# Performance work log

Hardware: AMD Instinct MI355X
Metric: run time of the kernel (lower is better)

## Reference

```python
import jax, jax.numpy as jnp
import numpy as np
import math

B, L, D, MAXL = 4, 4096, 1024, 16384


def setup_inputs() -> dict:
    key = jax.random.key(0)
    ks = jax.random.split(key, 12)
    s = 0.02
    def w(k, shape):
        return jax.random.normal(k, shape, jnp.float32) * s
    return {
        "x": jax.random.normal(ks[0], (B, L, D), jnp.float32),
        "pos_phases": jax.random.normal(ks[1], (MAXL, D), jnp.float32) * math.pi,
        "Wpv": w(ks[2], (D, D)), "bpv": jnp.zeros((D,), jnp.float32),
        "Wk": w(ks[3], (D, D)), "bk": jnp.zeros((D,), jnp.float32),
        "Wkv": w(ks[4], (D, D)), "bkv": jnp.zeros((D,), jnp.float32),
        "Wg1": w(ks[5], (2 * D, D)), "bg1": jnp.zeros((D,), jnp.float32),
        "Wg2": w(ks[6], (D, 1)), "bg2": jnp.zeros((1,), jnp.float32),
        "Wb1": w(ks[7], (D, D // 2)), "bb1": jnp.zeros((D // 2,), jnp.float32),
        "Wb2": w(ks[8], (D // 2, 2)), "bb2": jnp.zeros((2,), jnp.float32),
        "ln_g": jnp.ones((D,), jnp.float32), "ln_b": jnp.zeros((D,), jnp.float32),
        "Wo": w(ks[9], (D, D)), "bo": jnp.zeros((D,), jnp.float32),
    }


def _shift1(a):
    # torch.roll(a, 1, dims=1) with a[:, 0] = 0
    return jnp.concatenate([jnp.zeros_like(a[:, :1]), a[:, :-1]], axis=1)


def reference(x, pos_phases, Wpv, bpv, Wk, bk, Wkv, bkv, Wg1, bg1, Wg2, bg2,
              Wb1, bb1, Wb2, bb2, ln_g, ln_b, Wo, bo):
    Bq, Lq, Dq = x.shape
    sqrtD = jnp.sqrt(jnp.float32(Dq))

    # positional phasor memory
    pp = pos_phases[:Lq]                      # [L, D]
    pos_cos, pos_sin = jnp.cos(pp), jnp.sin(pp)
    pos_values = x @ Wpv + bpv                # [B, L, D]
    pos_mem_cos = jnp.cumsum(pos_cos * pos_values, axis=1)
    pos_mem_sin = jnp.cumsum(pos_sin * pos_values, axis=1)
    pos_ret = (pos_cos * pos_mem_cos + pos_sin * pos_mem_sin) / sqrtD

    # key-value phasor memory
    key_ph = jnp.tanh(x @ Wk + bk) * jnp.pi
    key_cos, key_sin = jnp.cos(key_ph), jnp.sin(key_ph)
    kv_values = x @ Wkv + bkv

    x_shifted = _shift1(x)
    gate_in = jnp.concatenate([x, x_shifted], axis=-1)       # [B, L, 2D]
    gh = jax.nn.gelu(gate_in @ Wg1 + bg1, approximate=False)
    value_gates = jax.nn.sigmoid(gh @ Wg2 + bg2)             # [B, L, 1]

    kc_s = _shift1(key_cos)
    ks_s = _shift1(key_sin)
    kv_mem_cos = jnp.cumsum(kc_s * kv_values * value_gates, axis=1)
    kv_mem_sin = jnp.cumsum(ks_s * kv_values * value_gates, axis=1)
    gate_cumsum = jnp.maximum(jnp.cumsum(value_gates, axis=1), 1.0)
    kv_ret = (key_cos * kv_mem_cos + key_sin * kv_mem_sin) / (jnp.sqrt(gate_cumsum) * sqrtD)

    # blend
    bh = jax.nn.gelu(x @ Wb1 + bb1, approximate=False)
    bw = jax.nn.softmax(bh @ Wb2 + bb2, axis=-1)             # [B, L, 2]
    blended = bw[..., 0:1] * pos_ret + bw[..., 1:2] * kv_ret

    # to_out: LayerNorm then Linear
    mu = jnp.mean(blended, axis=-1, keepdims=True)
    var = jnp.var(blended, axis=-1, keepdims=True)
    ln = (blended - mu) / jnp.sqrt(var + 1e-5) * ln_g + ln_b
    return x + ln @ Wo + bo
```

## Files before the change

### kernel.cpp

```cpp
#include <hip/hip_runtime.h>
#include <hip/hip_bf16.h>
#include <math.h>

using bf16 = __hip_bfloat16;
typedef __bf16 v8bf __attribute__((ext_vector_type(8)));
typedef float v4f __attribute__((ext_vector_type(4)));

#define B_ 4
#define L_ 4096
#define D_ 1024
#define M_ (B_*L_)
#define CCH 128
#define LCH (L_/CCH)
#define NF 3584

__device__ __forceinline__ float bf2f(bf16 v){ return __bfloat162float(v); }
__device__ __forceinline__ bf16 f2bf(float v){ return __float2bfloat16(v); }
__device__ __forceinline__ float us2f(ushort u){ union{unsigned u32; float f;}c; c.u32=((unsigned)u)<<16; return c.f; }
__device__ __forceinline__ ushort f2us(float v){ bf16 h=__float2bfloat16(v); return *(ushort*)&h; }
__device__ __forceinline__ float h2f(ushort u){ union{ushort s; _Float16 h;}c; c.s=u; return (float)c.h; }
__device__ __forceinline__ ushort f2h(float v){ union{ushort s; _Float16 h;}c; c.h=(_Float16)v; return c.s; }

__device__ __forceinline__ void g2l16(const void* g, void* l){
  __builtin_amdgcn_global_load_lds(
    (const __attribute__((address_space(1))) unsigned int*)g,
    (__attribute__((address_space(3))) unsigned int*)l, 16, 0, 0);
}

__global__ void k_zeroN(float* __restrict__ p, int n){
  int i = blockIdx.x*256 + threadIdx.x;
  if (i < n) p[i] = 0.0f;
}

__global__ void k_cvt(const float* __restrict__ in, bf16* __restrict__ out){
  int i = (blockIdx.x*256 + threadIdx.x)*4;
  float4 v = *(const float4*)(in + i);
  out[i]   = f2bf(v.x);
  out[i+1] = f2bf(v.y);
  out[i+2] = f2bf(v.z);
  out[i+3] = f2bf(v.w);
}

__global__ void k_cvt_pp(const float* __restrict__ in, ushort* __restrict__ out){
  int i = (blockIdx.x*256 + threadIdx.x)*4;
  float4 v = *(const float4*)(in + i);
  out[i]   = f2h(v.x);
  out[i+1] = f2h(v.y);
  out[i+2] = f2h(v.z);
  out[i+3] = f2h(v.w);
}

__global__ void k_ctr(const float* __restrict__ in, bf16* __restrict__ out, int R, int C){
  __shared__ float tile[32][33];
  int c0 = blockIdx.x*32, r0 = blockIdx.y*32;
  #pragma unroll
  for (int i=0;i<32;i+=8)
    tile[threadIdx.y+i][threadIdx.x] = in[(size_t)(r0+threadIdx.y+i)*C + c0+threadIdx.x];
  __syncthreads();
  #pragma unroll
  for (int i=0;i<32;i+=8)
    out[(size_t)(c0+threadIdx.y+i)*R + r0+threadIdx.x] = f2bf(tile[threadIdx.x][threadIdx.y+i]);
}

__global__ void k_pack_bias(const float* __restrict__ bpv, const float* __restrict__ bk,
                            const float* __restrict__ bkv, const float* __restrict__ bb1,
                            float* __restrict__ bf){
  int i = blockIdx.x*256 + threadIdx.x;
  float v;
  if (i < 1024) v = bpv[i];
  else if (i < 2048) v = bk[i-1024];
  else if (i < 3072) v = bkv[i-2048];
  else v = bb1[i-3072];
  bf[i] = v;
}

__device__ __forceinline__ float geluf(float v){
  return 0.5f*v*(1.0f + erff(v*0.70710678118654752f));
}
__device__ __forceinline__ float fast_tanh(float v){
  float a = fabsf(v);
  float e = __expf(-2.0f*a);
  float t = (1.0f - e)/(1.0f + e);
  return copysignf(t, v);
}

#define BM 256
#define BN 256
#define BK 64

template<int EPI, bool CONCAT>
__global__ __launch_bounds__(512) void k_gemm(
    const bf16* __restrict__ A, int lda,
    const bf16* __restrict__ Bt, int ldb,
    const float* __restrict__ bias,
    const bf16* __restrict__ zeros,
    bf16* __restrict__ o_pv, ushort* __restrict__ o_kp, bf16* __restrict__ o_kv,
    const float* __restrict__ Wv2, const float* __restrict__ Wb2f,
    float* __restrict__ gaccp, float* __restrict__ bwaccp,
    float* __restrict__ outf, const float* __restrict__ residf,
    int N, int Ktot)
{
  __shared__ __align__(16) ushort As[2*BM*BK];
  __shared__ __align__(16) ushort Bs[2*BN*BK];
  int tid = threadIdx.x;
  int lane = tid & 63, wave = tid >> 6;
  int wm = wave >> 2, wn = wave & 3;
  int nwgx = gridDim.x;
  int flat = blockIdx.y * nwgx + blockIdx.x;
  int chunk = (nwgx * gridDim.y) >> 3;
  int newid = (flat & 7) * chunk + (flat >> 3);
  int bn = (newid % nwgx) * BN, bm = (newid / nwgx) * BM;

  v4f zero = {0.f,0.f,0.f,0.f};
  v4f acc[8][4];
  #pragma unroll
  for (int i=0;i<8;i++)
    #pragma unroll
    for (int j=0;j<4;j++) acc[i][j] = zero;

  int mr = lane & 15, g4 = lane >> 4;
  int srow = lane >> 3, sseg = lane & 7;
  int swzs = (sseg ^ srow) * 8;

  auto stage_half = [&](int t, int which){
    int buf = t & 1;
    int kk = t * BK;
    bool isA = (which==0) || (which==3);
    int rbase = (which==0 || which==1) ? 0 : 128;
    ushort* dst = (isA ? As : Bs) + buf*(BM*BK);
    #pragma unroll
    for (int p=0;p<2;p++){
      int r = rbase + p*64 + wave*8 + srow;
      const bf16* src;
      if (isA){
        if (!CONCAT || kk < D_) {
          src = A + (size_t)(bm + r)*lda + (size_t)kk + swzs;
        } else {
          int m = bm + r;
          int l = m & (L_-1);
          src = (l==0) ? (zeros + swzs)
                       : (A + (size_t)(m-1)*lda + (size_t)(kk - D_) + swzs);
        }
      } else {
        src = Bt + (size_t)(bn + r)*ldb + (size_t)kk + swzs;
      }
      g2l16(src, dst + (size_t)(rbase + p*64 + wave*8)*BK);
    }
  };

  auto lds_a = [&](const ushort* Ab, int ih, int i, int ks)->v8bf{
    int row = ih*128 + wm*64 + i*16 + mr;
    int off = row*128 + ((ks*64 + g4*16) ^ ((mr&7)<<4));
    return *(const v8bf*)((const char*)Ab + off);
  };
  auto lds_b = [&](const ushort* Bb, int jh, int j, int ks)->v8bf{
    int row = jh*128 + wn*32 + j*16 + mr;
    int off = row*128 + ((ks*64 + g4*16) ^ ((mr&7)<<4));
    return *(const v8bf*)((const char*)Bb + off);
  };

  int nt = Ktot / BK;
  stage_half(0,0); stage_half(0,1); stage_half(0,2); stage_half(0,3);
  __syncthreads();

  v8bf a[4][2];
  v8bf b[2][2][2];

  for (int t=0; t<nt; ++t){
    const ushort* Ab = As + (t&1)*(BM*BK);
    const ushort* Bb = Bs + (t&1)*(BM*BK);
    bool more = (t+1 < nt);

    if (more){
      stage_half(t+1, 0); stage_half(t+1, 1);
      stage_half(t+1, 2); stage_half(t+1, 3);
    }

    #pragma unroll
    for (int i=0;i<4;i++){ a[i][0] = lds_a(Ab,0,i,0); a[i][1] = lds_a(Ab,0,i,1); }
    #pragma unroll
    for (int j=0;j<2;j++){ b[0][j][0] = lds_b(Bb,0,j,0); b[0][j][1] = lds_b(Bb,0,j,1); }
    __builtin_amdgcn_s_setprio(1);
    #pragma unroll
    for (int i=0;i<4;i++)
      #pragma unroll
      for (int j=0;j<2;j++){
        acc[i][j] = __builtin_amdgcn_mfma_f32_16x16x32_bf16(a[i][0], b[0][j][0], acc[i][j], 0,0,0);
        acc[i][j] = __builtin_amdgcn_mfma_f32_16x16x32_bf16(a[i][1], b[0][j][1], acc[i][j], 0,0,0);
      }
    __builtin_amdgcn_s_setprio(0);

    #pragma unroll
    for (int j=0;j<2;j++){ b[1][j][0] = lds_b(Bb,1,j,0); b[1][j][1] = lds_b(Bb,1,j,1); }
    __builtin_amdgcn_s_setprio(1);
    #pragma unroll
    for (int i=0;i<4;i++)
      #pragma unroll
      for (int j=0;j<2;j++){
        acc[i][2+j] = __builtin_amdgcn_mfma_f32_16x16x32_bf16(a[i][0], b[1][j][0], acc[i][2+j], 0,0,0);
        acc[i][2+j] = __builtin_amdgcn_mfma_f32_16x16x32_bf16(a[i][1], b[1][j][1], acc[i][2+j], 0,0,0);
      }
    __builtin_amdgcn_s_setprio(0);

    #pragma unroll
    for (int i=0;i<4;i++){ a[i][0] = lds_a(Ab,1,i,0); a[i][1] = lds_a(Ab,1,i,1); }
    __builtin_amdgcn_s_setprio(1);
    #pragma unroll
    for (int i=0;i<4;i++)
      #pragma unroll
      for (int j=0;j<2;j++){
        acc[4+i][2+j] = __builtin_amdgcn_mfma_f32_16x16x32_bf16(a[i][0], b[1][j][0], acc[4+i][2+j], 0,0,0);
        acc[4+i][2+j] = __builtin_amdgcn_mfma_f32_16x16x32_bf16(a[i][1], b[1][j][1], acc[4+i][2+j], 0,0,0);
      }
    __builtin_amdgcn_s_setprio(0);

    __builtin_amdgcn_s_setprio(1);
    #pragma unroll
    for (int i=0;i<4;i++)
      #pragma unroll
      for (int j=0;j<2;j++){
        acc[4+i][j] = __builtin_amdgcn_mfma_f32_16x16x32_bf16(a[i][0], b[0][j][0], acc[4+i][j], 0,0,0);
        acc[4+i][j] = __builtin_amdgcn_mfma_f32_16x16x32_bf16(a[i][1], b[0][j][1], acc[4+i][j], 0,0,0);
      }
    __builtin_amdgcn_s_setprio(0);

    __syncthreads();
  }

  int lr = lane >> 4, lc = lane & 15;
  if (EPI == 3){
    #pragma unroll
    for (int ai=0;ai<8;ai++){
      #pragma unroll
      for (int bj=0;bj<4;bj++){
        int col  = bn + (bj>>1)*128 + wn*32 + (bj&1)*16 + lc;
        int row0 = bm + (ai>>2)*128 + wm*64 + (ai&3)*16 + lr*4;
        float bias_v = bias[col];
        #pragma unroll
        for (int rr=0; rr<4; rr++){
          size_t idx = (size_t)(row0+rr)*N + col;
          outf[idx] = acc[ai][bj][rr] + bias_v + residf[idx];
        }
      }
    }
  } else if (EPI == 2){
    #pragma unroll
    for (int ai=0;ai<8;ai++){
      float red[4] = {0.f,0.f,0.f,0.f};
      #pragma unroll
      for (int bj=0;bj<4;bj++){
        int col = bn + (bj>>1)*128 + wn*32 + (bj&1)*16 + lc;
        float bias_v = bias[col];
        float wv = Wv2[col];
        #pragma unroll
        for (int rr=0; rr<4; rr++){
          float v = acc[ai][bj][rr] + bias_v;
          red[rr] += geluf(v) * wv;
        }
      }
      int row0 = bm + (ai>>2)*128 + wm*64 + (ai&3)*16 + lr*4;
      #pragma unroll
      for (int rr=0; rr<4; rr++){
        float r = red[rr];
        r += __shfl_xor(r,1); r += __shfl_xor(r,2);
        r += __shfl_xor(r,4); r += __shfl_xor(r,8);
        if (lc == 0) atomicAdd(&gaccp[row0+rr], r);
      }
    }
  } else {
    if (bn < 3072){
      #pragma unroll
      for (int ai=0;ai<8;ai++){
        #pragma unroll
        for (int bj=0;bj<4;bj++){
          int col  = bn + (bj>>1)*128 + wn*32 + (bj&1)*16 + lc;
          int row0 = bm + (ai>>2)*128 + wm*64 + (ai&3)*16 + lr*4;
          float bias_v = bias[col];
          #pragma unroll
          for (int rr=0; rr<4; rr++){
            int row = row0 + rr;
            float v = acc[ai][bj][rr] + bias_v;
            if (bn < 1024) {
              o_pv[(size_t)row*1024 + col] = f2bf(v);
            } else if (bn < 2048) {
              float kp = fast_tanh(v) * 3.14159265358979323846f;
              o_kp[(size_t)row*1024 + (col-1024)] = f2h(kp);
            } else {
              o_kv[(size_t)row*1024 + (col-2048)] = f2bf(v);
            }
          }
        }
      }
    } else {
      #pragma unroll
      for (int ai=0;ai<8;ai++){
        float r0[4] = {0.f,0.f,0.f,0.f};
        float r1[4] = {0.f,0.f,0.f,0.f};
        #pragma unroll
        for (int bj=0;bj<4;bj++){
          int col = bn + (bj>>1)*128 + wn*32 + (bj&1)*16 + lc;
          float bias_v = bias[col];
          int kb = col - 3072;
          float w0 = Wb2f[kb*2], w1 = Wb2f[kb*2+1];
          #pragma unroll
          for (int rr=0; rr<4; rr++){
            float v = acc[ai][bj][rr] + bias_v;
            float gl = geluf(v);
            r0[rr] += gl*w0;
            r1[rr] += gl*w1;
          }
        }
        int row0 = bm + (ai>>2)*128 + wm*64 + (ai&3)*16 + lr*4;
        #pragma unroll
        for (int rr=0; rr<4; rr++){
          float a2 = r0[rr], b2 = r1[rr];
          a2 += __shfl_xor(a2,1); a2 += __shfl_xor(a2,2); a2 += __shfl_xor(a2,4); a2 += __shfl_xor(a2,8);
          b2 += __shfl_xor(b2,1); b2 += __shfl_xor(b2,2); b2 += __shfl_xor(b2,4); b2 += __shfl_xor(b2,8);
          if (lc == 0){
            atomicAdd(&bwaccp[(size_t)(row0+rr)*2],   a2);
            atomicAdd(&bwaccp[(size_t)(row0+rr)*2+1], b2);
          }
        }
      }
    }
  }
}

__global__ __launch_bounds__(1024) void k_gscan(const float* __restrict__ gacc,
                                                const float* __restrict__ bg2,
                                                float* __restrict__ g, float* __restrict__ gc){
  __shared__ float sa[1024];
  int b = blockIdx.x, tid = threadIdx.x;
  int base = b*L_ + tid*4;
  float bb = bg2[0];
  float v0 = 1.f/(1.f+__expf(-(gacc[base]   + bb)));
  float v1 = 1.f/(1.f+__expf(-(gacc[base+1] + bb)));
  float v2 = 1.f/(1.f+__expf(-(gacc[base+2] + bb)));
  float v3 = 1.f/(1.f+__expf(-(gacc[base+3] + bb)));
  float s0 = v0, s1 = s0+v1, s2 = s1+v2, s3 = s2+v3;
  sa[tid] = s3; __syncthreads();
  for (int o=1;o<1024;o<<=1){
    float t = sa[tid] + ((tid>=o) ? sa[tid-o] : 0.f);
    __syncthreads();
    sa[tid] = t;
    __syncthreads();
  }
  float ex = sa[tid] - s3;
  g[base]=v0; g[base+1]=v1; g[base+2]=v2; g[base+3]=v3;
  gc[base]=ex+s0; gc[base+1]=ex+s1; gc[base+2]=ex+s2; gc[base+3]=ex+s3;
}

__global__ void k_finishbw(const float* __restrict__ bwacc, const float* __restrict__ bb2,
                           float2* __restrict__ bw){
  int t = blockIdx.x*256 + threadIdx.x;
  float a = bwacc[(size_t)t*2]   + bb2[0];
  float b = bwacc[(size_t)t*2+1] + bb2[1];
  float m = fmaxf(a,b);
  float e0 = __expf(a-m), e1 = __expf(b-m);
  float inv = 1.0f/(e0+e1);
  bw[t] = make_float2(e0*inv, e1*inv);
}

__global__ void k_scan_partial(const bf16* __restrict__ PV, const bf16* __restrict__ KV,
                               const ushort* __restrict__ KP, const float* __restrict__ g,
                               const ushort* __restrict__ ppH, float* __restrict__ PS){
  int tid = threadIdx.x;
  int d0 = tid*4;
  int j = blockIdx.x, b = blockIdx.y;
  int l0 = j*LCH;
  float pkc[4]={0,0,0,0}, pks[4]={0,0,0,0};
  if (l0 > 0){
    size_t pidx = ((size_t)b*L_ + l0-1)*D_ + d0;
    ushort4 up = *(const ushort4*)(KP+pidx);
    float ph0=h2f(up.x), ph1=h2f(up.y), ph2=h2f(up.z), ph3=h2f(up.w);
    __sincosf(ph0,&pks[0],&pkc[0]); __sincosf(ph1,&pks[1],&pkc[1]);
    __sincosf(ph2,&pks[2],&pkc[2]); __sincosf(ph3,&pks[3],&pkc[3]);
  }
  float p0[4]={0,0,0,0}, p1[4]={0,0,0,0}, p2[4]={0,0,0,0}, p3[4]={0,0,0,0};
  for (int l=l0; l<l0+LCH; l++){
    size_t idx = ((size_t)b*L_ + l)*D_ + d0;
    ushort4 upv = *(const ushort4*)(PV+idx);
    ushort4 ukv = *(const ushort4*)(KV+idx);
    ushort4 ukp = *(const ushort4*)(KP+idx);
    ushort4 upp = *(const ushort4*)(ppH + (size_t)l*D_ + d0);
    float gl = g[b*L_ + l];
    float pvv[4]={us2f(upv.x),us2f(upv.y),us2f(upv.z),us2f(upv.w)};
    float kvv[4]={us2f(ukv.x),us2f(ukv.y),us2f(ukv.z),us2f(ukv.w)};
    float kpv[4]={h2f(ukp.x),h2f(ukp.y),h2f(ukp.z),h2f(ukp.w)};
    float phv[4]={h2f(upp.x),h2f(upp.y),h2f(upp.z),h2f(upp.w)};
    #pragma unroll
    for (int c=0;c<4;c++){
      float sn, cs; __sincosf(phv[c], &sn, &cs);
      float kc, ks; __sincosf(kpv[c], &ks, &kc);
      float kvg = kvv[c]*gl;
      p0[c] += cs*pvv[c]; p1[c] += sn*pvv[c];
      p2[c] += pkc[c]*kvg; p3[c] += pks[c]*kvg;
      pkc[c]=kc; pks[c]=ks;
    }
  }
  size_t base = ((size_t)b*CCH + j)*D_ + d0;
  size_t plane = (size_t)B_*CCH*D_;
  #pragma unroll
  for (int c=0;c<4;c++){
    PS[0*plane + base + c] = p0[c];
    PS[1*plane + base + c] = p1[c];
    PS[2*plane + base + c] = p2[c];
    PS[3*plane + base + c] = p3[c];
  }
}

__global__ void k_prefix(float* __restrict__ PS){
  int idx = blockIdx.x*256 + threadIdx.x;
  int q = idx >> 12;
  int rem = idx & 4095;
  int b = rem >> 10, d = rem & 1023;
  size_t plane = (size_t)B_*CCH*D_;
  float* base = PS + (size_t)q*plane + (size_t)b*CCH*D_ + d;
  float s = 0.0f;
  for (int j=0;j<CCH;j+=4){
    float v0 = base[(size_t)(j  )*D_];
    float v1 = base[(size_t)(j+1)*D_];
    float v2 = base[(size_t)(j+2)*D_];
    float v3 = base[(size_t)(j+3)*D_];
    base[(size_t)(j  )*D_] = s; s += v0;
    base[(size_t)(j+1)*D_] = s; s += v1;
    base[(size_t)(j+2)*D_] = s; s += v2;
    base[(size_t)(j+3)*D_] = s; s += v3;
  }
}

__global__ void k_scan_apply(const bf16* __restrict__ PV, const bf16* __restrict__ KV,
                             const ushort* __restrict__ KP, const float* __restrict__ g,
                             const ushort* __restrict__ ppH, const float* __restrict__ PS,
                             const float* __restrict__ gc, const float2* __restrict__ bw,
                             const float* __restrict__ ln_g, const float* __restrict__ ln_b,
                             bf16* __restrict__ LNB){
  __shared__ float sA[4], sB[4];
  int tid = threadIdx.x;
  int d0 = tid*4;
  int j = blockIdx.x, b = blockIdx.y;
  int l0 = j*LCH;
  size_t base = ((size_t)b*CCH + j)*D_ + d0;
  size_t plane = (size_t)B_*CCH*D_;
  float mc[4], ms[4], kcm[4], ksm[4];
  #pragma unroll
  for (int c=0;c<4;c++){
    mc[c]  = PS[0*plane+base+c]; ms[c]  = PS[1*plane+base+c];
    kcm[c] = PS[2*plane+base+c]; ksm[c] = PS[3*plane+base+c];
  }
  float pkc[4]={0,0,0,0}, pks[4]={0,0,0,0};
  if (l0 > 0){
    size_t pidx = ((size_t)b*L_ + l0-1)*D_ + d0;
    ushort4 up = *(const ushort4*)(KP+pidx);
    float ph0=h2f(up.x), ph1=h2f(up.y), ph2=h2f(up.z), ph3=h2f(up.w);
    __sincosf(ph0,&pks[0],&pkc[0]); __sincosf(ph1,&pks[1],&pkc[1]);
    __sincosf(ph2,&pks[2],&pkc[2]); __sincosf(ph3,&pks[3],&pkc[3]);
  }
  float4 gv = *(const float4*)&ln_g[d0];
  float4 bv = *(const float4*)&ln_b[d0];
  int wv = tid >> 6, ln = tid & 63;
  for (int l=l0; l<l0+LCH; l++){
    size_t idx = ((size_t)b*L_ + l)*D_ + d0;
    ushort4 upv = *(const ushort4*)(PV+idx);
    ushort4 ukv = *(const ushort4*)(KV+idx);
    ushort4 ukp = *(const ushort4*)(KP+idx);
    ushort4 upp = *(const ushort4*)(ppH + (size_t)l*D_ + d0);
    float gl = g[b*L_ + l];
    float gcv = fmaxf(gc[b*L_+l], 1.0f);
    float rs = 0.03125f * rsqrtf(gcv);
    float2 w = bw[b*L_+l];
    float pvv[4]={us2f(upv.x),us2f(upv.y),us2f(upv.z),us2f(upv.w)};
    float kvv[4]={us2f(ukv.x),us2f(ukv.y),us2f(ukv.z),us2f(ukv.w)};
    float kpv[4]={h2f(ukp.x),h2f(ukp.y),h2f(ukp.z),h2f(ukp.w)};
    float phv[4]={h2f(upp.x),h2f(upp.y),h2f(upp.z),h2f(upp.w)};
    float bl[4];
    #pragma unroll
    for (int c=0;c<4;c++){
      float sn, cs; __sincosf(phv[c], &sn, &cs);
      float kc, ks; __sincosf(kpv[c], &ks, &kc);
      mc[c] += cs*pvv[c]; ms[c] += sn*pvv[c];
      float pos_ret = (cs*mc[c] + sn*ms[c]) * 0.03125f;
      float kvg = kvv[c]*gl;
      kcm[c] += pkc[c]*kvg; ksm[c] += pks[c]*kvg;
      float kv_ret = (kc*kcm[c] + ks*ksm[c]) * rs;
      bl[c] = w.x*pos_ret + w.y*kv_ret;
      pkc[c]=kc; pks[c]=ks;
    }
    float s  = bl[0]+bl[1]+bl[2]+bl[3];
    float s2 = bl[0]*bl[0]+bl[1]*bl[1]+bl[2]*bl[2]+bl[3]*bl[3];
    #pragma unroll
    for (int o=1;o<64;o<<=1){ s += __shfl_xor(s,o); s2 += __shfl_xor(s2,o); }
    if (ln == 0){ sA[wv] = s; sB[wv] = s2; }
    __syncthreads();
    float ts  = sA[0]+sA[1]+sA[2]+sA[3];
    float ts2 = sB[0]+sB[1]+sB[2]+sB[3];
    __syncthreads();
    float mu   = ts * (1.0f/D_);
    float var  = ts2 * (1.0f/D_) - mu*mu;
    float rstd = rsqrtf(var + 1e-5f);
    ushort4 ou;
    ou.x = f2us((bl[0]-mu)*rstd*gv.x + bv.x);
    ou.y = f2us((bl[1]-mu)*rstd*gv.y + bv.y);
    ou.z = f2us((bl[2]-mu)*rstd*gv.z + bv.z);
    ou.w = f2us((bl[3]-mu)*rstd*gv.w + bv.w);
    *(ushort4*)((ushort*)LNB + idx) = ou;
  }
}

extern "C" void kernel_launch(void* const* d_in, const int* in_sizes, int n_in,
                              void* d_out, int out_size, void* d_ws, size_t ws_size,
                              hipStream_t stream) {
  const float* x     = (const float*)d_in[0];
  const float* phases= (const float*)d_in[1];
  const float* Wpv   = (const float*)d_in[2];
  const float* bpv   = (const float*)d_in[3];
  const float* Wk    = (const float*)d_in[4];
  const float* bk    = (const float*)d_in[5];
  const float* Wkv   = (const float*)d_in[6];
  const float* bkv   = (const float*)d_in[7];
  const float* Wg1   = (const float*)d_in[8];
  const float* bg1   = (const float*)d_in[9];
  const float* Wg2   = (const float*)d_in[10];
  const float* bg2   = (const float*)d_in[11];
  const float* Wb1   = (const float*)d_in[12];
  const float* bb1   = (const float*)d_in[13];
  const float* Wb2   = (const float*)d_in[14];
  const float* bb2   = (const float*)d_in[15];
  const float* ln_g  = (const float*)d_in[16];
  const float* ln_b  = (const float*)d_in[17];
  const float* Wo    = (const float*)d_in[18];
  const float* bo    = (const float*)d_in[19];
  float* out = (float*)d_out;

  char* ws = (char*)d_ws;
  size_t off = 0;
  auto alloc = [&](size_t bytes)->char*{
    char* p = ws + off; off += (bytes + 255) & ~(size_t)255; return p;
  };
  bf16*  xb   = (bf16*)alloc((size_t)M_*D_*2);
  bf16*  WfT  = (bf16*)alloc((size_t)NF*D_*2);
  bf16*  Wg1T = (bf16*)alloc((size_t)D_*2*D_*2);
  bf16*  WoT  = (bf16*)alloc((size_t)D_*D_*2);
  bf16*  PV   = (bf16*)alloc((size_t)M_*D_*2);
  bf16*  KV   = (bf16*)alloc((size_t)M_*D_*2);
  ushort* KP  = (ushort*)alloc((size_t)M_*D_*2);
  ushort* ppH = (ushort*)alloc((size_t)L_*D_*2);
  bf16*  LNB  = (bf16*)alloc((size_t)M_*D_*2);
  float* gbuf  = (float*)alloc((size_t)M_*4);
  float* gcbuf = (float*)alloc((size_t)M_*4);
  float2* bwbuf= (float2*)alloc((size_t)M_*8);
  float* PS    = (float*)alloc((size_t)4*B_*CCH*D_*4);
  float* biasF = (float*)alloc((size_t)NF*4);
  float* gacc  = (float*)alloc((size_t)M_*4);
  float* bwacc = (float*)alloc((size_t)M_*2*4);
  bf16*  zeros = (bf16*)alloc(256);
  int nzero = (M_ + 2*M_ + 64);

  k_zeroN<<<(nzero+255)/256,256,0,stream>>>(gacc, nzero);
  k_cvt<<<(M_*D_)/1024, 256, 0, stream>>>(x, xb);
  k_cvt_pp<<<(L_*D_)/1024, 256, 0, stream>>>(phases, ppH);

  dim3 tb(32,8);
  k_ctr<<<dim3(D_/32, D_/32), tb, 0, stream>>>(Wpv, WfT,                       D_, D_);
  k_ctr<<<dim3(D_/32, D_/32), tb, 0, stream>>>(Wk,  WfT + (size_t)1024*D_,     D_, D_);
  k_ctr<<<dim3(D_/32, D_/32), tb, 0, stream>>>(Wkv, WfT + (size_t)2048*D_,     D_, D_);
  k_ctr<<<dim3((D_/2)/32, D_/32), tb, 0, stream>>>(Wb1, WfT + (size_t)3072*D_, D_, D_/2);
  k_ctr<<<dim3(D_/32, 2*D_/32), tb, 0, stream>>>(Wg1, Wg1T, 2*D_, D_);
  k_ctr<<<dim3(D_/32, D_/32), tb, 0, stream>>>(Wo,  WoT,  D_, D_);
  k_pack_bias<<<NF/256,256,0,stream>>>(bpv, bk, bkv, bb1, biasF);

  k_gemm<4,false><<<dim3(NF/BN, M_/BM),512,0,stream>>>(
      xb, D_, WfT, D_, biasF, zeros, PV, KP, KV, nullptr, Wb2, nullptr, bwacc,
      nullptr, nullptr, NF, D_);
  k_gemm<2,true><<<dim3(D_/BN, M_/BM),512,0,stream>>>(
      xb, D_, Wg1T, 2*D_, bg1, zeros, nullptr, nullptr, nullptr, Wg2, nullptr, gacc, nullptr,
      nullptr, nullptr, D_, 2*D_);
  k_gscan<<<B_,1024,0,stream>>>(gacc, bg2, gbuf, gcbuf);
  k_finishbw<<<M_/256,256,0,stream>>>(bwacc, bb2, bwbuf);
  dim3 sg(CCH, B_);
  k_scan_partial<<<sg,256,0,stream>>>(PV, KV, KP, gbuf, ppH, PS);
  k_prefix<<<(4*B_*D_)/256,256,0,stream>>>(PS);
  k_scan_apply<<<sg,256,0,stream>>>(PV, KV, KP, gbuf, ppH, PS, gcbuf, bwbuf, ln_g, ln_b, LNB);
  k_gemm<3,false><<<dim3(D_/BN, M_/BM),512,0,stream>>>(
      LNB, D_, WoT, D_, bo, zeros, nullptr, nullptr, nullptr, nullptr, nullptr, nullptr, nullptr,
      out, x, D_, D_);
}
```

Before: 597.2 us.

## Load GEMM B operand fragments directly from global memory instead of LDS

Removes the shared-memory staging buffer for the weight (B) tile and has each wave read its MFMA B fragments straight from global memory, while A keeps the double-buffered LDS path, now staged in one call per tile. This halves LDS usage, which may allow more occupancy, and drops the B staging traffic. In exchange, B fragments are re-fetched by every wave row that shares them, become synchronous global loads on the critical path of the MFMA loop, and lose cross-wave reuse through LDS.

```diff
diff --git a/kernel.cpp b/kernel.cpp
--- a/kernel.cpp
+++ b/kernel.cpp
@@ -101,7 +101,6 @@
     int N, int Ktot)
 {
   __shared__ __align__(16) ushort As[2*BM*BK];
-  __shared__ __align__(16) ushort Bs[2*BN*BK];
   int tid = threadIdx.x;
   int lane = tid & 63, wave = tid >> 6;
   int wm = wave >> 2, wn = wave & 3;
@@ -122,29 +121,22 @@
   int srow = lane >> 3, sseg = lane & 7;
   int swzs = (sseg ^ srow) * 8;
 
-  auto stage_half = [&](int t, int which){
-    int buf = t & 1;
+  auto stage_A = [&](int t, int buf){
     int kk = t * BK;
-    bool isA = (which==0) || (which==3);
-    int rbase = (which==0 || which==1) ? 0 : 128;
-    ushort* dst = (isA ? As : Bs) + buf*(BM*BK);
-    #pragma unroll
-    for (int p=0;p<2;p++){
-      int r = rbase + p*64 + wave*8 + srow;
+    ushort* dst = As + buf*(BM*BK);
+    #pragma unroll
+    for (int p=0;p<4;p++){
+      int r = p*64 + wave*8 + srow;
       const bf16* src;
-      if (isA){
-        if (!CONCAT || kk < D_) {
-          src = A + (size_t)(bm + r)*lda + (size_t)kk + swzs;
-        } else {
-          int m = bm + r;
-          int l = m & (L_-1);
-          src = (l==0) ? (zeros + swzs)
-                       : (A + (size_t)(m-1)*lda + (size_t)(kk - D_) + swzs);
-        }
+      if (!CONCAT || kk < D_) {
+        src = A + (size_t)(bm + r)*lda + (size_t)kk + swzs;
       } else {
-        src = Bt + (size_t)(bn + r)*ldb + (size_t)kk + swzs;
-      }
-      g2l16(src, dst + (size_t)(rbase + p*64 + wave*8)*BK);
+        int m = bm + r;
+        int l = m & (L_-1);
+        src = (l==0) ? (zeros + swzs)
+                     : (A + (size_t)(m-1)*lda + (size_t)(kk - D_) + swzs);
+      }
+      g2l16(src, dst + (size_t)(p*64 + wave*8)*BK);
     }
   };
 
@@ -153,14 +145,13 @@
     int off = row*128 + ((ks*64 + g4*16) ^ ((mr&7)<<4));
     return *(const v8bf*)((const char*)Ab + off);
   };
-  auto lds_b = [&](const ushort* Bb, int jh, int j, int ks)->v8bf{
-    int row = jh*128 + wn*32 + j*16 + mr;
-    int off = row*128 + ((ks*64 + g4*16) ^ ((mr&7)<<4));
-    return *(const v8bf*)((const char*)Bb + off);
+  auto glb_b = [&](int t, int jh, int j, int ks)->v8bf{
+    size_t col = (size_t)(bn + jh*128 + wn*32 + j*16 + mr);
+    return *(const v8bf*)(Bt + col*ldb + (size_t)t*BK + ks*32 + g4*8);
   };
 
   int nt = Ktot / BK;
-  stage_half(0,0); stage_half(0,1); stage_half(0,2); stage_half(0,3);
+  stage_A(0, 0);
   __syncthreads();
 
   v8bf a[4][2];
@@ -168,18 +159,14 @@
 
   for (int t=0; t<nt; ++t){
     const ushort* Ab = As + (t&1)*(BM*BK);
-    const ushort* Bb = Bs + (t&1)*(BM*BK);
     bool more = (t+1 < nt);
 
-    if (more){
-      stage_half(t+1, 0); stage_half(t+1, 1);
-      stage_half(t+1, 2); stage_half(t+1, 3);
-    }
+    if (more) stage_A(t+1, (t+1)&1);
 
     #pragma unroll
     for (int i=0;i<4;i++){ a[i][0] = lds_a(Ab,0,i,0); a[i][1] = lds_a(Ab,0,i,1); }
     #pragma unroll
-    for (int j=0;j<2;j++){ b[0][j][0] = lds_b(Bb,0,j,0); b[0][j][1] = lds_b(Bb,0,j,1); }
+    for (int j=0;j<2;j++){ b[0][j][0] = glb_b(t,0,j,0); b[0][j][1] = glb_b(t,0,j,1); }
     __builtin_amdgcn_s_setprio(1);
     #pragma unroll
     for (int i=0;i<4;i++)
@@ -191,7 +178,7 @@
     __builtin_amdgcn_s_setprio(0);
 
     #pragma unroll
-    for (int j=0;j<2;j++){ b[1][j][0] = lds_b(Bb,1,j,0); b[1][j][1] = lds_b(Bb,1,j,1); }
+    for (int j=0;j<2;j++){ b[1][j][0] = glb_b(t,1,j,0); b[1][j][1] = glb_b(t,1,j,1); }
     __builtin_amdgcn_s_setprio(1);
     #pragma unroll
     for (int i=0;i<4;i++)
```

Measured after the change: 878.5 us. 47.1% more time.
